# Optimization experiments

Measured on AMD Instinct MI355X. Metric: run time of the kernel, lower is better.

Reference implementation:

```python
import jax, jax.numpy as jnp
import numpy as np

NUM_CHANNELS = 512
B_DIM = 64
C_DIM = 16
N = 512
FEAT = NUM_CHANNELS * 4 * 4  # 8192


def setup_inputs() -> dict:
    key = jax.random.key(0)
    k1, k2 = jax.random.split(key)
    inp = jax.random.normal(k1, (N, NUM_CHANNELS, 4, 4), dtype=jnp.float32)
    T = jax.random.normal(k2, (FEAT, B_DIM * C_DIM), dtype=jnp.float32) * 0.1
    return {"inp": inp, "T": T}


def reference(inp, T):
    x = inp.reshape(-1, FEAT)                      # (N, 8192)
    M = (x @ T).reshape(-1, B_DIM, C_DIM)          # (N, B, C)
    # pairwise L1 distance over C: (N, N, B)
    dist = jnp.sum(jnp.abs(M[:, None, :, :] - M[None, :, :, :]), axis=-1)
    o = jnp.sum(jnp.exp(-dist), axis=1)            # (N, B)
    return jnp.concatenate((x, o), axis=1)         # (N, 8192 + B)
```

## Files before the change

kernel.cpp:

```cpp
#include <hip/hip_runtime.h>
#include <hip/hip_bf16.h>

#define NROWS 512
#define FEAT  8192
#define BDIM  64
#define CDIM  16
#define MCOLS 1024
#define OUTC  8256
#define KSPLIT 4
#define KCHUNK (FEAT / KSPLIT)

typedef __bf16 bf16x8 __attribute__((ext_vector_type(8)));
typedef float  floatx4 __attribute__((ext_vector_type(4)));

static __device__ inline unsigned short f2bf(float f) {
    unsigned int x = __builtin_bit_cast(unsigned int, f);
    unsigned int r = (x + 0x7FFFu + ((x >> 16) & 1u)) >> 16;
    return (unsigned short)r;
}

__global__ __launch_bounds__(256) void convx_kernel(const float* __restrict__ x,
                                                    unsigned short* __restrict__ xb,
                                                    float* __restrict__ out) {
    int gid = blockIdx.x * 256 + threadIdx.x;
    float4 v = *(const float4*)(x + (size_t)gid * 4);
    ushort4 u;
    u.x = f2bf(v.x); u.y = f2bf(v.y); u.z = f2bf(v.z); u.w = f2bf(v.w);
    *(ushort4*)(xb + (size_t)gid * 4) = u;
    int row  = gid >> 11;
    int col4 = gid & 2047;
    *(float4*)(out + (size_t)row * OUTC + col4 * 4) = v;
}

__global__ __launch_bounds__(256) void convt_kernel(const float* __restrict__ T,
                                                    unsigned short* __restrict__ Tt) {
    int bid = blockIdx.x;
    int kt = bid & 255;
    int nt = bid >> 8;
    __shared__ float lds[32][33];
    int tx = threadIdx.x & 31;
    int ty = threadIdx.x >> 5;
#pragma unroll
    for (int p = 0; p < 4; ++p) {
        int kk = ty + p * 8;
        lds[kk][tx] = T[(size_t)(kt * 32 + kk) * MCOLS + nt * 32 + tx];
    }
    __syncthreads();
#pragma unroll
    for (int p = 0; p < 4; ++p) {
        int nn = ty + p * 8;
        Tt[(size_t)(nt * 32 + nn) * FEAT + kt * 32 + tx] = f2bf(lds[tx][nn]);
    }
}

__global__ __launch_bounds__(256) void gemm_kernel(const unsigned short* __restrict__ xb,
                                                   const unsigned short* __restrict__ Tt,
                                                   float* __restrict__ Mp) {
    int bid = blockIdx.x;
    int mt = bid & 7;
    int nt = (bid >> 3) & 15;
    int ks = bid >> 7;
    int m0 = mt * 64, n0 = nt * 64, kbase = ks * KCHUNK;

    __shared__ __align__(16) unsigned short ldsA[64][40];
    __shared__ __align__(16) unsigned short ldsB[64][40];

    int t = threadIdx.x;
    int lrow = t >> 2;
    int lc8  = t & 3;
    const unsigned short* gA = xb + (size_t)(m0 + lrow) * FEAT + kbase + lc8 * 8;
    const unsigned short* gB = Tt + (size_t)(n0 + lrow) * FEAT + kbase + lc8 * 8;

    int lane = t & 63, w = t >> 6;
    int fm = lane & 15, fq = lane >> 4;
    const unsigned short* pA  = &ldsA[w * 16 + fm][fq * 8];
    const unsigned short* pB0 = &ldsB[ 0 + fm][fq * 8];
    const unsigned short* pB1 = &ldsB[16 + fm][fq * 8];
    const unsigned short* pB2 = &ldsB[32 + fm][fq * 8];
    const unsigned short* pB3 = &ldsB[48 + fm][fq * 8];

    floatx4 acc0 = {}, acc1 = {}, acc2 = {}, acc3 = {};

    for (int kk = 0; kk < KCHUNK; kk += 32) {
        uint4 a = *(const uint4*)(gA + kk);
        uint4 b = *(const uint4*)(gB + kk);
        __syncthreads();
        *(uint4*)&ldsA[lrow][lc8 * 8] = a;
        *(uint4*)&ldsB[lrow][lc8 * 8] = b;
        __syncthreads();
        bf16x8 af = *(const bf16x8*)pA;
        acc0 = __builtin_amdgcn_mfma_f32_16x16x32_bf16(af, *(const bf16x8*)pB0, acc0, 0, 0, 0);
        acc1 = __builtin_amdgcn_mfma_f32_16x16x32_bf16(af, *(const bf16x8*)pB1, acc1, 0, 0, 0);
        acc2 = __builtin_amdgcn_mfma_f32_16x16x32_bf16(af, *(const bf16x8*)pB2, acc2, 0, 0, 0);
        acc3 = __builtin_amdgcn_mfma_f32_16x16x32_bf16(af, *(const bf16x8*)pB3, acc3, 0, 0, 0);
    }

    float* outp = Mp + (size_t)ks * NROWS * MCOLS;
    int row = m0 + w * 16 + fq * 4;
    int col = n0 + fm;
#pragma unroll
    for (int r = 0; r < 4; ++r) {
        outp[(size_t)(row + r) * MCOLS + col +  0] = acc0[r];
        outp[(size_t)(row + r) * MCOLS + col + 16] = acc1[r];
        outp[(size_t)(row + r) * MCOLS + col + 32] = acc2[r];
        outp[(size_t)(row + r) * MCOLS + col + 48] = acc3[r];
    }
}

__global__ __launch_bounds__(256) void pairwise_kernel(const float* __restrict__ Mp,
                                                       float* __restrict__ out) {
    int b  = blockIdx.x & 63;
    int it = blockIdx.x >> 6;
    __shared__ __align__(16) float ldsM[NROWS][CDIM];
    __shared__ float partial[4][64];

    int t = threadIdx.x;
#pragma unroll
    for (int p = 0; p < 8; ++p) {
        int idx = t + p * 256;
        int j = idx >> 2, c4 = idx & 3;
        const float* base = Mp + (size_t)j * MCOLS + b * CDIM + c4 * 4;
        float4 v0 = *(const float4*)(base);
        float4 v1 = *(const float4*)(base + 1 * NROWS * MCOLS);
        float4 v2 = *(const float4*)(base + 2 * NROWS * MCOLS);
        float4 v3 = *(const float4*)(base + 3 * NROWS * MCOLS);
        float4 s;
        s.x = v0.x + v1.x + v2.x + v3.x;
        s.y = v0.y + v1.y + v2.y + v3.y;
        s.z = v0.z + v1.z + v2.z + v3.z;
        s.w = v0.w + v1.w + v2.w + v3.w;
        *(float4*)&ldsM[j][c4 * 4] = s;
    }
    __syncthreads();

    int lane = t & 63, w = t >> 6;
    int i = it * 64 + lane;
    float mi[CDIM];
#pragma unroll
    for (int c = 0; c < CDIM; ++c) mi[c] = ldsM[i][c];

    float acc = 0.0f;
    int j0 = w * 128;
    for (int jj = j0; jj < j0 + 128; ++jj) {
        float d = 0.0f;
#pragma unroll
        for (int c = 0; c < CDIM; ++c) d += fabsf(mi[c] - ldsM[jj][c]);
        acc += __expf(-d);
    }
    partial[w][lane] = acc;
    __syncthreads();
    if (w == 0) {
        float o = partial[0][lane] + partial[1][lane] + partial[2][lane] + partial[3][lane];
        out[(size_t)i * OUTC + FEAT + b] = o;
    }
}

extern "C" void kernel_launch(void* const* d_in, const int* in_sizes, int n_in,
                              void* d_out, int out_size, void* d_ws, size_t ws_size,
                              hipStream_t stream) {
    const float* x = (const float*)d_in[0];
    const float* T = (const float*)d_in[1];
    float* out = (float*)d_out;

    unsigned short* xb = (unsigned short*)d_ws;
    unsigned short* Tt = (unsigned short*)((char*)d_ws + (8u << 20));
    float*          Mp = (float*)((char*)d_ws + (24u << 20));

    convx_kernel<<<4096, 256, 0, stream>>>(x, xb, out);
    convt_kernel<<<8192, 256, 0, stream>>>(T, Tt);
    gemm_kernel<<<512, 256, 0, stream>>>(xb, Tt, Mp);
    pairwise_kernel<<<512, 256, 0, stream>>>(Mp, out);
}
```

Baseline: 150.8 us.

## Fuse prep kernels, enlarge GEMM tiles with direct LDS loads, add split-K reduce

Merges the x conversion and T transpose into one launch, with a 64x64 transpose tile that writes vectorized bf16 stores. The GEMM moves to 128x128 tiles with a 4x4 MFMA accumulator grid per wave, swizzled LDS, and global_load_lds direct loads, and the split-K factor rises to 16. A separate reduce kernel sums the 16 partials before the pairwise kernel, whose LDS rows are padded to 20 floats. The aim is more compute per loaded byte and fewer launches, at the cost of more partial-sum traffic (16 partial M copies written and read) plus one extra kernel.

```diff
diff --git a/kernel.cpp b/kernel.cpp
--- a/kernel.cpp
+++ b/kernel.cpp
@@ -1,5 +1,4 @@
 #include <hip/hip_runtime.h>
-#include <hip/hip_bf16.h>
 
 #define NROWS 512
 #define FEAT  8192
@@ -7,129 +6,157 @@
 #define CDIM  16
 #define MCOLS 1024
 #define OUTC  8256
-#define KSPLIT 4
+#define KSPLIT 16
 #define KCHUNK (FEAT / KSPLIT)
+#define MSIZE  (NROWS * MCOLS)
 
 typedef __bf16 bf16x8 __attribute__((ext_vector_type(8)));
 typedef float  floatx4 __attribute__((ext_vector_type(4)));
 
-static __device__ inline unsigned short f2bf(float f) {
+#define AS1 __attribute__((address_space(1)))
+#define AS3 __attribute__((address_space(3)))
+
+static __device__ __forceinline__ void gload16(const void* g, void* l) {
+    __builtin_amdgcn_global_load_lds((AS1 void*)(g), (AS3 void*)(l), 16, 0, 0);
+}
+
+static __device__ __forceinline__ unsigned short f2bf(float f) {
     unsigned int x = __builtin_bit_cast(unsigned int, f);
     unsigned int r = (x + 0x7FFFu + ((x >> 16) & 1u)) >> 16;
     return (unsigned short)r;
 }
 
-__global__ __launch_bounds__(256) void convx_kernel(const float* __restrict__ x,
-                                                    unsigned short* __restrict__ xb,
-                                                    float* __restrict__ out) {
+__global__ __launch_bounds__(256) void prep_kernel(const float* __restrict__ x,
+                                                   const float* __restrict__ T,
+                                                   unsigned short* __restrict__ xb,
+                                                   unsigned short* __restrict__ Tt,
+                                                   float* __restrict__ out) {
+    __shared__ float lds[64][65];
+    int bid = blockIdx.x, t = threadIdx.x;
+    if (bid < 4096) {
+        int gid = bid * 256 + t;
+        float4 v = *(const float4*)(x + (size_t)gid * 4);
+        ushort4 u;
+        u.x = f2bf(v.x); u.y = f2bf(v.y); u.z = f2bf(v.z); u.w = f2bf(v.w);
+        *(ushort4*)(xb + (size_t)gid * 4) = u;
+        int row = gid >> 11, col4 = gid & 2047;
+        *(float4*)(out + (size_t)row * OUTC + col4 * 4) = v;
+    } else {
+        int b2 = bid - 4096;
+        int kt = b2 & 127, nt = b2 >> 7;
+        int kk = t >> 2, q = t & 3;
+#pragma unroll
+        for (int p = 0; p < 4; ++p) {
+            int c4 = q + p * 4;
+            float4 v = *(const float4*)(T + (size_t)(kt * 64 + kk) * MCOLS + nt * 64 + c4 * 4);
+            lds[kk][c4 * 4 + 0] = v.x; lds[kk][c4 * 4 + 1] = v.y;
+            lds[kk][c4 * 4 + 2] = v.z; lds[kk][c4 * 4 + 3] = v.w;
+        }
+        __syncthreads();
+        int nr = t >> 2, ck = t & 3;
+        unsigned int w[8];
+#pragma unroll
+        for (int j = 0; j < 8; ++j) {
+            unsigned int lo = f2bf(lds[ck * 16 + j * 2 + 0][nr]);
+            unsigned int hi = f2bf(lds[ck * 16 + j * 2 + 1][nr]);
+            w[j] = lo | (hi << 16);
+        }
+        uint4* dst = (uint4*)(Tt + (size_t)(nt * 64 + nr) * FEAT + kt * 64 + ck * 16);
+        dst[0] = make_uint4(w[0], w[1], w[2], w[3]);
+        dst[1] = make_uint4(w[4], w[5], w[6], w[7]);
+    }
+}
+
+__global__ __launch_bounds__(256, 2) void gemm_kernel(const unsigned short* __restrict__ xb,
+                                                      const unsigned short* __restrict__ Tt,
+                                                      float* __restrict__ Mp) {
+    __shared__ __align__(16) unsigned short ldsA[128 * 32];
+    __shared__ __align__(16) unsigned short ldsB[128 * 32];
+
+    int bid = blockIdx.x;
+    int mt = bid & 3, nt = (bid >> 2) & 7, ks = bid >> 5;
+    int m0 = mt * 128, n0 = nt * 128, kbase = ks * KCHUNK;
+    int t = threadIdx.x, w = t >> 6, l = t & 63;
+
+    int r0 = w * 32 + (l >> 2);
+    int c  = (l & 3) ^ ((r0 >> 1) & 3);
+    const unsigned short* gA0 = xb + (size_t)(m0 + r0) * FEAT + kbase + c * 8;
+    const unsigned short* gB0 = Tt + (size_t)(n0 + r0) * FEAT + kbase + c * 8;
+    unsigned short* lA0 = &ldsA[w * 1024];
+    unsigned short* lA1 = &ldsA[w * 1024 + 512];
+    unsigned short* lB0 = &ldsB[w * 1024];
+    unsigned short* lB1 = &ldsB[w * 1024 + 512];
+
+    int wr = w >> 1, wc = w & 1, fm = l & 15, fq = l >> 4;
+    int swz = (fm >> 1) & 3;
+    const unsigned short* pa[4];
+    const unsigned short* pb[4];
+#pragma unroll
+    for (int a = 0; a < 4; ++a)
+        pa[a] = &ldsA[(wr * 64 + a * 16 + fm) * 32 + ((fq ^ swz) * 8)];
+#pragma unroll
+    for (int b = 0; b < 4; ++b)
+        pb[b] = &ldsB[(wc * 64 + b * 16 + fm) * 32 + ((fq ^ swz) * 8)];
+
+    floatx4 acc[4][4] = {};
+
+    for (int kk = 0; kk < KCHUNK; kk += 32) {
+        if (kk) __syncthreads();
+        gload16(gA0 + kk,             lA0);
+        gload16(gA0 + 16 * FEAT + kk, lA1);
+        gload16(gB0 + kk,             lB0);
+        gload16(gB0 + 16 * FEAT + kk, lB1);
+        __syncthreads();
+        bf16x8 af[4], bfr[4];
+#pragma unroll
+        for (int a = 0; a < 4; ++a) af[a] = *(const bf16x8*)pa[a];
+#pragma unroll
+        for (int b = 0; b < 4; ++b) bfr[b] = *(const bf16x8*)pb[b];
+#pragma unroll
+        for (int a = 0; a < 4; ++a)
+#pragma unroll
+            for (int b = 0; b < 4; ++b)
+                acc[a][b] = __builtin_amdgcn_mfma_f32_16x16x32_bf16(af[a], bfr[b], acc[a][b], 0, 0, 0);
+    }
+
+    float* outp = Mp + (size_t)ks * MSIZE;
+    int gr0 = m0 + wr * 64, gc0 = n0 + wc * 64;
+#pragma unroll
+    for (int a = 0; a < 4; ++a)
+#pragma unroll
+        for (int r = 0; r < 4; ++r) {
+            int row = gr0 + a * 16 + fq * 4 + r;
+#pragma unroll
+            for (int b = 0; b < 4; ++b)
+                outp[(size_t)row * MCOLS + gc0 + b * 16 + fm] = acc[a][b][r];
+        }
+}
+
+__global__ __launch_bounds__(256) void reduce_kernel(const float* __restrict__ Mp,
+                                                     float* __restrict__ Ms) {
     int gid = blockIdx.x * 256 + threadIdx.x;
-    float4 v = *(const float4*)(x + (size_t)gid * 4);
-    ushort4 u;
-    u.x = f2bf(v.x); u.y = f2bf(v.y); u.z = f2bf(v.z); u.w = f2bf(v.w);
-    *(ushort4*)(xb + (size_t)gid * 4) = u;
-    int row  = gid >> 11;
-    int col4 = gid & 2047;
-    *(float4*)(out + (size_t)row * OUTC + col4 * 4) = v;
-}
-
-__global__ __launch_bounds__(256) void convt_kernel(const float* __restrict__ T,
-                                                    unsigned short* __restrict__ Tt) {
-    int bid = blockIdx.x;
-    int kt = bid & 255;
-    int nt = bid >> 8;
-    __shared__ float lds[32][33];
-    int tx = threadIdx.x & 31;
-    int ty = threadIdx.x >> 5;
-#pragma unroll
-    for (int p = 0; p < 4; ++p) {
-        int kk = ty + p * 8;
-        lds[kk][tx] = T[(size_t)(kt * 32 + kk) * MCOLS + nt * 32 + tx];
-    }
-    __syncthreads();
-#pragma unroll
-    for (int p = 0; p < 4; ++p) {
-        int nn = ty + p * 8;
-        Tt[(size_t)(nt * 32 + nn) * FEAT + kt * 32 + tx] = f2bf(lds[tx][nn]);
-    }
-}
-
-__global__ __launch_bounds__(256) void gemm_kernel(const unsigned short* __restrict__ xb,
-                                                   const unsigned short* __restrict__ Tt,
-                                                   float* __restrict__ Mp) {
-    int bid = blockIdx.x;
-    int mt = bid & 7;
-    int nt = (bid >> 3) & 15;
-    int ks = bid >> 7;
-    int m0 = mt * 64, n0 = nt * 64, kbase = ks * KCHUNK;
-
-    __shared__ __align__(16) unsigned short ldsA[64][40];
-    __shared__ __align__(16) unsigned short ldsB[64][40];
-
-    int t = threadIdx.x;
-    int lrow = t >> 2;
-    int lc8  = t & 3;
-    const unsigned short* gA = xb + (size_t)(m0 + lrow) * FEAT + kbase + lc8 * 8;
-    const unsigned short* gB = Tt + (size_t)(n0 + lrow) * FEAT + kbase + lc8 * 8;
-
-    int lane = t & 63, w = t >> 6;
-    int fm = lane & 15, fq = lane >> 4;
-    const unsigned short* pA  = &ldsA[w * 16 + fm][fq * 8];
-    const unsigned short* pB0 = &ldsB[ 0 + fm][fq * 8];
-    const unsigned short* pB1 = &ldsB[16 + fm][fq * 8];
-    const unsigned short* pB2 = &ldsB[32 + fm][fq * 8];
-    const unsigned short* pB3 = &ldsB[48 + fm][fq * 8];
-
-    floatx4 acc0 = {}, acc1 = {}, acc2 = {}, acc3 = {};
-
-    for (int kk = 0; kk < KCHUNK; kk += 32) {
-        uint4 a = *(const uint4*)(gA + kk);
-        uint4 b = *(const uint4*)(gB + kk);
-        __syncthreads();
-        *(uint4*)&ldsA[lrow][lc8 * 8] = a;
-        *(uint4*)&ldsB[lrow][lc8 * 8] = b;
-        __syncthreads();
-        bf16x8 af = *(const bf16x8*)pA;
-        acc0 = __builtin_amdgcn_mfma_f32_16x16x32_bf16(af, *(const bf16x8*)pB0, acc0, 0, 0, 0);
-        acc1 = __builtin_amdgcn_mfma_f32_16x16x32_bf16(af, *(const bf16x8*)pB1, acc1, 0, 0, 0);
-        acc2 = __builtin_amdgcn_mfma_f32_16x16x32_bf16(af, *(const bf16x8*)pB2, acc2, 0, 0, 0);
-        acc3 = __builtin_amdgcn_mfma_f32_16x16x32_bf16(af, *(const bf16x8*)pB3, acc3, 0, 0, 0);
-    }
-
-    float* outp = Mp + (size_t)ks * NROWS * MCOLS;
-    int row = m0 + w * 16 + fq * 4;
-    int col = n0 + fm;
-#pragma unroll
-    for (int r = 0; r < 4; ++r) {
-        outp[(size_t)(row + r) * MCOLS + col +  0] = acc0[r];
-        outp[(size_t)(row + r) * MCOLS + col + 16] = acc1[r];
-        outp[(size_t)(row + r) * MCOLS + col + 32] = acc2[r];
-        outp[(size_t)(row + r) * MCOLS + col + 48] = acc3[r];
-    }
-}
-
-__global__ __launch_bounds__(256) void pairwise_kernel(const float* __restrict__ Mp,
+    const float4* p = (const float4*)Mp;
+    float4 s = p[gid];
+#pragma unroll
+    for (int k = 1; k < KSPLIT; ++k) {
+        float4 v = p[(size_t)k * (MSIZE / 4) + gid];
+        s.x += v.x; s.y += v.y; s.z += v.z; s.w += v.w;
+    }
+    ((float4*)Ms)[gid] = s;
+}
+
+__global__ __launch_bounds__(256) void pairwise_kernel(const float* __restrict__ Ms,
                                                        float* __restrict__ out) {
-    int b  = blockIdx.x & 63;
-    int it = blockIdx.x >> 6;
-    __shared__ __align__(16) float ldsM[NROWS][CDIM];
+    __shared__ float ldsM[NROWS * 20];
     __shared__ float partial[4][64];
-
+    int b = blockIdx.x & 63, it = blockIdx.x >> 6;
     int t = threadIdx.x;
 #pragma unroll
     for (int p = 0; p < 8; ++p) {
         int idx = t + p * 256;
         int j = idx >> 2, c4 = idx & 3;
-        const float* base = Mp + (size_t)j * MCOLS + b * CDIM + c4 * 4;
-        float4 v0 = *(const float4*)(base);
-        float4 v1 = *(const float4*)(base + 1 * NROWS * MCOLS);
-        float4 v2 = *(const float4*)(base + 2 * NROWS * MCOLS);
-        float4 v3 = *(const float4*)(base + 3 * NROWS * MCOLS);
-        float4 s;
-        s.x = v0.x + v1.x + v2.x + v3.x;
-        s.y = v0.y + v1.y + v2.y + v3.y;
-        s.z = v0.z + v1.z + v2.z + v3.z;
-        s.w = v0.w + v1.w + v2.w + v3.w;
-        *(float4*)&ldsM[j][c4 * 4] = s;
+        float4 v = *(const float4*)(Ms + (size_t)j * MCOLS + b * CDIM + c4 * 4);
+        *(float4*)&ldsM[j * 20 + c4 * 4] = v;
     }
     __syncthreads();
 
@@ -137,14 +164,13 @@
     int i = it * 64 + lane;
     float mi[CDIM];
 #pragma unroll
-    for (int c = 0; c < CDIM; ++c) mi[c] = ldsM[i][c];
+    for (int cc = 0; cc < CDIM; ++cc) mi[cc] = ldsM[i * 20 + cc];
 
     float acc = 0.0f;
-    int j0 = w * 128;
-    for (int jj = j0; jj < j0 + 128; ++jj) {
+    for (int jj = w * 128; jj < w * 128 + 128; ++jj) {
         float d = 0.0f;
 #pragma unroll
-        for (int c = 0; c < CDIM; ++c) d += fabsf(mi[c] - ldsM[jj][c]);
+        for (int cc = 0; cc < CDIM; ++cc) d += fabsf(mi[cc] - ldsM[jj * 20 + cc]);
         acc += __expf(-d);
     }
     partial[w][lane] = acc;
@@ -165,9 +191,10 @@
     unsigned short* xb = (unsigned short*)d_ws;
     unsigned short* Tt = (unsigned short*)((char*)d_ws + (8u << 20));
     float*          Mp = (float*)((char*)d_ws + (24u << 20));
-
-    convx_kernel<<<4096, 256, 0, stream>>>(x, xb, out);
-    convt_kernel<<<8192, 256, 0, stream>>>(T, Tt);
+    float*          Ms = (float*)((char*)d_ws + (56u << 20));
+
+    prep_kernel<<<6144, 256, 0, stream>>>(x, T, xb, Tt, out);
     gemm_kernel<<<512, 256, 0, stream>>>(xb, Tt, Mp);
-    pairwise_kernel<<<512, 256, 0, stream>>>(Mp, out);
-}
+    reduce_kernel<<<512, 256, 0, stream>>>(Mp, Ms);
+    pairwise_kernel<<<512, 256, 0, stream>>>(Ms, out);
+}
```

Measured after the change: 137.1 us. 9.0% less time.
